# Optimization experiments

Hardware: AMD Instinct MI355X
Metric: run time of the kernel (lower is better)

## Reference

```python
import jax, jax.numpy as jnp
import numpy as np

NUM_NODE_TYPES = 8
HIDDEN = 64
D = 4
N_NODES = 100000
N_EDGES = 3200000
LN_EPS = 1e-5


def setup_inputs() -> dict:
    key = jax.random.key(0)
    ks = jax.random.split(key, 8)
    total_in = 2 * NUM_NODE_TYPES
    out_dim = D * D
    x = jax.random.normal(ks[0], (N_NODES, 16), dtype=jnp.float32)
    edge_index = jax.random.randint(ks[1], (2, N_EDGES), 0, N_NODES, dtype=jnp.int64)
    node_types = jax.random.randint(ks[2], (N_NODES,), 0, NUM_NODE_TYPES, dtype=jnp.int64)
    # LayerNorm params
    ln_g = jnp.ones((total_in,), dtype=jnp.float32)
    ln_b = jnp.zeros((total_in,), dtype=jnp.float32)
    # Linear layers (kaiming-ish init)
    W1 = jax.random.normal(ks[3], (total_in, HIDDEN), dtype=jnp.float32) * (1.0 / np.sqrt(total_in))
    b1 = jnp.zeros((HIDDEN,), dtype=jnp.float32)
    W2 = jax.random.normal(ks[4], (HIDDEN, out_dim), dtype=jnp.float32) * (1.0 / np.sqrt(HIDDEN))
    b2 = jnp.zeros((out_dim,), dtype=jnp.float32)
    return {"x": x, "edge_index": edge_index, "node_types": node_types,
            "ln_g": ln_g, "ln_b": ln_b, "W1": W1, "b1": b1, "W2": W2, "b2": b2}


def reference(x, edge_index, node_types, ln_g, ln_b, W1, b1, W2, b2):
    row, col = edge_index[0], edge_index[1]
    # one-hot node types then per-edge gather of src/tgt types
    onehot = jax.nn.one_hot(node_types, NUM_NODE_TYPES, dtype=jnp.float32)  # [N, T]
    h = jnp.concatenate([onehot[row], onehot[col]], axis=-1)  # [E, 2T]
    # LayerNorm
    mu = jnp.mean(h, axis=-1, keepdims=True)
    var = jnp.mean(jnp.square(h - mu), axis=-1, keepdims=True)
    hn = (h - mu) * jax.lax.rsqrt(var + LN_EPS) * ln_g + ln_b
    # MLP
    h1 = jax.nn.relu(hn @ W1 + b1)          # [E, HIDDEN]
    h_sheaf = (h1 @ W2 + b2).reshape(-1, D, D)  # [E, d, d]
    attention_maps = jax.nn.softmax(h_sheaf, axis=-1)
    sheaf_maps = jnp.eye(D, dtype=h_sheaf.dtype)[None] - attention_maps
    return sheaf_maps
```

## Files before the change

kernel.cpp:

```cpp
#include <hip/hip_runtime.h>
#include <math.h>

#define NUM_T   8
#define TIN     16
#define HID     64
#define OUTD    16
#define LN_EPS  1e-5f

#define N_PACK_U32  12500
#define PACK_BLOCKS 49

typedef float f32x4 __attribute__((ext_vector_type(4)));

__global__ __launch_bounds__(256) void
prep_kernel(const int* __restrict__ ntypes, int n_nodes,
            const float* __restrict__ ln_g,
            const float* __restrict__ ln_b,
            const float* __restrict__ W1,
            const float* __restrict__ b1,
            const float* __restrict__ W2,
            const float* __restrict__ b2,
            f32x4* __restrict__ table4,
            unsigned int* __restrict__ packed)
{
    const int t = threadIdx.x;

    if (blockIdx.x < PACK_BLOCKS) {
        const int g = blockIdx.x * 256 + t;
        if (g < N_PACK_U32) {
            unsigned int w = 0;
            int n0 = g * 8;
            #pragma unroll
            for (int j = 0; j < 8; ++j) {
                int n = n0 + j;
                unsigned int ty = (n < n_nodes) ? (unsigned int)ntypes[n] : 0u;
                w |= (ty & 7u) << (j * 4);
            }
            packed[g] = w;
        }
        return;
    }

    if (t >= 64) return;
    const int p  = blockIdx.x - PACK_BLOCKS;
    const int ts = p >> 3;
    const int tt = p & 7;
    const int k  = t;

    const float mu = 2.0f / 16.0f;
    float var = 0.0f;
    #pragma unroll
    for (int j = 0; j < TIN; ++j) {
        float h = (j == ts || j == (8 + tt)) ? 1.0f : 0.0f;
        float d = h - mu;
        var += d * d;
    }
    var *= (1.0f / 16.0f);
    const float inv = rsqrtf(var + LN_EPS);

    float a = b1[k];
    #pragma unroll
    for (int j = 0; j < TIN; ++j) {
        float h  = (j == ts || j == (8 + tt)) ? 1.0f : 0.0f;
        float hn = (h - mu) * inv * ln_g[j] + ln_b[j];
        a += hn * W1[j * HID + k];
    }
    a = fmaxf(a, 0.0f);

    const f32x4* W2v = (const f32x4*)W2;
    f32x4 w0 = W2v[k * 4 + 0], w1 = W2v[k * 4 + 1],
          w2 = W2v[k * 4 + 2], w3 = W2v[k * 4 + 3];

    float s[OUTD];
    #pragma unroll
    for (int i = 0; i < 4; ++i) {
        s[0 + i]  = a * w0[i];
        s[4 + i]  = a * w1[i];
        s[8 + i]  = a * w2[i];
        s[12 + i] = a * w3[i];
    }
    #pragma unroll
    for (int o = 0; o < OUTD; ++o) {
        s[o] += __shfl_xor(s[o], 1);
        s[o] += __shfl_xor(s[o], 2);
        s[o] += __shfl_xor(s[o], 4);
        s[o] += __shfl_xor(s[o], 8);
        s[o] += __shfl_xor(s[o], 16);
        s[o] += __shfl_xor(s[o], 32);
        s[o] += b2[o];
    }

    if (t < 4) {
        const int r = t;
        float s0 = s[4*r+0], s1 = s[4*r+1], s2 = s[4*r+2], s3 = s[4*r+3];
        float m  = fmaxf(fmaxf(s0, s1), fmaxf(s2, s3));
        float e0 = expf(s0 - m), e1 = expf(s1 - m),
              e2 = expf(s2 - m), e3 = expf(s3 - m);
        float rs = 1.0f / (e0 + e1 + e2 + e3);
        f32x4 outv;
        outv.x = (r == 0 ? 1.0f : 0.0f) - e0 * rs;
        outv.y = (r == 1 ? 1.0f : 0.0f) - e1 * rs;
        outv.z = (r == 2 ? 1.0f : 0.0f) - e2 * rs;
        outv.w = (r == 3 ? 1.0f : 0.0f) - e3 * rs;
        table4[p * 4 + r] = outv;
    }
}

__global__ __launch_bounds__(1024) void
scatter_edges_kernel(const int* __restrict__ row,
                     const int* __restrict__ col,
                     const unsigned int* __restrict__ packed,
                     const f32x4* __restrict__ table4,
                     f32x4* __restrict__ out4,
                     int E)
{
    __shared__ f32x4 lds_table[64 * 5];
    __shared__ unsigned int nt_lds[N_PACK_U32];

    const int t = threadIdx.x;

    if (t < 256) {
        int p = t >> 2, q = t & 3;
        lds_table[p * 5 + q] = table4[t];
    }
    {
        const uint4* s4 = (const uint4*)packed;
        uint4* d4 = (uint4*)nt_lds;
        for (int i = t; i < N_PACK_U32 / 4; i += 1024) d4[i] = s4[i];
    }
    __syncthreads();

    const int lane = t & 63;
    const int wid  = t >> 6;
    const int q    = lane & 3;
    const int sub  = lane >> 2;
    const int stride = gridDim.x * 1024;

    int base = blockIdx.x * 1024 + wid * 64;
    if (base >= E) return;

    int pair;
    {
        int e  = base + lane;
        int ec = (e < E) ? e : (E - 1);
        int r = row[ec];
        int c = col[ec];
        unsigned int tr = (nt_lds[r >> 3] >> ((r & 7) * 4)) & 7u;
        unsigned int tc = (nt_lds[c >> 3] >> ((c & 7) * 4)) & 7u;
        pair = (int)((tr << 3) | tc);
    }

    while (base < E) {
        const int nbase = base + stride;
        const bool have_next = (nbase < E);

        int rn = 0, cn = 0;
        if (have_next) {
            int en  = nbase + lane;
            int enc = (en < E) ? en : (E - 1);
            rn = row[enc];
            cn = col[enc];
        }

        #pragma unroll
        for (int j = 0; j < 4; ++j) {
            int src = j * 16 + sub;
            int pj  = __shfl(pair, src, 64);
            int ej  = base + src;
            if (ej < E) {
                out4[ej * 4 + q] = lds_table[pj * 5 + q];
            }
        }

        if (have_next) {
            unsigned int tr = (nt_lds[rn >> 3] >> ((rn & 7) * 4)) & 7u;
            unsigned int tc = (nt_lds[cn >> 3] >> ((cn & 7) * 4)) & 7u;
            pair = (int)((tr << 3) | tc);
        }
        base = nbase;
    }
}

extern "C" void kernel_launch(void* const* d_in, const int* in_sizes, int n_in,
                              void* d_out, int out_size, void* d_ws, size_t ws_size,
                              hipStream_t stream)
{
    const int*   edge_index = (const int*)d_in[1];
    const int*   ntypes     = (const int*)d_in[2];
    const float* ln_g       = (const float*)d_in[3];
    const float* ln_b       = (const float*)d_in[4];
    const float* W1         = (const float*)d_in[5];
    const float* b1         = (const float*)d_in[6];
    const float* W2         = (const float*)d_in[7];
    const float* b2         = (const float*)d_in[8];

    const int E = in_sizes[1] / 2;
    const int N = in_sizes[2];

    f32x4*        table4 = (f32x4*)d_ws;
    unsigned int* packed = (unsigned int*)((char*)d_ws + 4096);

    prep_kernel<<<PACK_BLOCKS + 64, 256, 0, stream>>>(
        ntypes, N, ln_g, ln_b, W1, b1, W2, b2, table4, packed);

    const int blocks = 512;
    scatter_edges_kernel<<<blocks, 1024, 0, stream>>>(
        edge_index, edge_index + E, packed,
        table4, (f32x4*)d_out, E);
}
```

Before: 46.23 us.

## Add vectorized exact-chunk scatter path with int4 index loads and packed pair shuffles

Adds a fast path, used when the edge count is a multiple of 256, that processes 256-edge chunks per wavefront. Row and column indices are read with int4 loads, and four type pairs are packed into one register so a single shuffle serves four edges. The path drops bounds checks, uses a 256-block grid and keeps next-chunk prefetching. The old kernel becomes a simpler generic fallback without prefetch, and the fast path depends on the edge count's divisibility.

```diff
diff --git a/kernel.cpp b/kernel.cpp
--- a/kernel.cpp
+++ b/kernel.cpp
@@ -107,12 +107,89 @@
 }
 
 __global__ __launch_bounds__(1024) void
-scatter_edges_kernel(const int* __restrict__ row,
-                     const int* __restrict__ col,
-                     const unsigned int* __restrict__ packed,
-                     const f32x4* __restrict__ table4,
-                     f32x4* __restrict__ out4,
-                     int E)
+scatter_edges_exact(const int* __restrict__ row,
+                    const int* __restrict__ col,
+                    const unsigned int* __restrict__ packed,
+                    const f32x4* __restrict__ table4,
+                    f32x4* __restrict__ out4,
+                    int nchunks)
+{
+    __shared__ f32x4 lds_table[64 * 5];
+    __shared__ unsigned int nt_lds[N_PACK_U32];
+
+    const int t = threadIdx.x;
+
+    if (t < 256) {
+        int p = t >> 2, q = t & 3;
+        lds_table[p * 5 + q] = table4[t];
+    }
+    {
+        const uint4* s4 = (const uint4*)packed;
+        uint4* d4 = (uint4*)nt_lds;
+        for (int i = t; i < N_PACK_U32 / 4; i += 1024) d4[i] = s4[i];
+    }
+    __syncthreads();
+
+    const int lane = t & 63;
+    const int wid  = t >> 6;
+    const int q        = lane & 3;
+    const int selshift = 8 * ((lane >> 2) & 3);
+    const int lhi      = lane >> 4;
+
+    const int4* row4 = (const int4*)row;
+    const int4* col4 = (const int4*)col;
+
+    int ci = blockIdx.x * 16 + wid;
+    const int stride = gridDim.x * 16;
+    if (ci >= nchunks) return;
+
+    int4 rv = row4[ci * 64 + lane];
+    int4 cv = col4[ci * 64 + lane];
+
+    while (true) {
+        const int nci = ci + stride;
+        const bool have_next = (nci < nchunks);
+
+        int4 rvn, cvn;
+        if (have_next) {
+            rvn = row4[nci * 64 + lane];
+            cvn = col4[nci * 64 + lane];
+        }
+
+        unsigned int pp = 0;
+        {
+            int rr[4] = {rv.x, rv.y, rv.z, rv.w};
+            int cc[4] = {cv.x, cv.y, cv.z, cv.w};
+            #pragma unroll
+            for (int j = 0; j < 4; ++j) {
+                unsigned int tr = (nt_lds[rr[j] >> 3] >> ((rr[j] & 7) * 4)) & 7u;
+                unsigned int tc = (nt_lds[cc[j] >> 3] >> ((cc[j] & 7) * 4)) & 7u;
+                pp |= ((tr << 3) | tc) << (8 * j);
+            }
+        }
+
+        const int base4 = ci * 1024;
+        #pragma unroll
+        for (int i = 0; i < 16; ++i) {
+            unsigned int ppj = (unsigned int)__shfl((int)pp, 4 * i + lhi, 64);
+            int pj = (int)((ppj >> selshift) & 63u);
+            out4[base4 + i * 64 + lane] = lds_table[pj * 5 + q];
+        }
+
+        if (!have_next) break;
+        ci = nci;
+        rv = rvn;
+        cv = cvn;
+    }
+}
+
+__global__ __launch_bounds__(1024) void
+scatter_edges_generic(const int* __restrict__ row,
+                      const int* __restrict__ col,
+                      const unsigned int* __restrict__ packed,
+                      const f32x4* __restrict__ table4,
+                      f32x4* __restrict__ out4,
+                      int E)
 {
     __shared__ f32x4 lds_table[64 * 5];
     __shared__ unsigned int nt_lds[N_PACK_U32];
@@ -136,48 +213,22 @@
     const int sub  = lane >> 2;
     const int stride = gridDim.x * 1024;
 
-    int base = blockIdx.x * 1024 + wid * 64;
-    if (base >= E) return;
-
-    int pair;
-    {
+    for (int base = blockIdx.x * 1024 + wid * 64; base < E; base += stride) {
         int e  = base + lane;
         int ec = (e < E) ? e : (E - 1);
         int r = row[ec];
         int c = col[ec];
         unsigned int tr = (nt_lds[r >> 3] >> ((r & 7) * 4)) & 7u;
         unsigned int tc = (nt_lds[c >> 3] >> ((c & 7) * 4)) & 7u;
-        pair = (int)((tr << 3) | tc);
-    }
-
-    while (base < E) {
-        const int nbase = base + stride;
-        const bool have_next = (nbase < E);
-
-        int rn = 0, cn = 0;
-        if (have_next) {
-            int en  = nbase + lane;
-            int enc = (en < E) ? en : (E - 1);
-            rn = row[enc];
-            cn = col[enc];
-        }
+        int pair = (int)((tr << 3) | tc);
 
         #pragma unroll
         for (int j = 0; j < 4; ++j) {
             int src = j * 16 + sub;
             int pj  = __shfl(pair, src, 64);
             int ej  = base + src;
-            if (ej < E) {
-                out4[ej * 4 + q] = lds_table[pj * 5 + q];
-            }
-        }
-
-        if (have_next) {
-            unsigned int tr = (nt_lds[rn >> 3] >> ((rn & 7) * 4)) & 7u;
-            unsigned int tc = (nt_lds[cn >> 3] >> ((cn & 7) * 4)) & 7u;
-            pair = (int)((tr << 3) | tc);
-        }
-        base = nbase;
+            if (ej < E) out4[ej * 4 + q] = lds_table[pj * 5 + q];
+        }
     }
 }
 
@@ -203,8 +254,11 @@
     prep_kernel<<<PACK_BLOCKS + 64, 256, 0, stream>>>(
         ntypes, N, ln_g, ln_b, W1, b1, W2, b2, table4, packed);
 
-    const int blocks = 512;
-    scatter_edges_kernel<<<blocks, 1024, 0, stream>>>(
-        edge_index, edge_index + E, packed,
-        table4, (f32x4*)d_out, E);
-}
+    if ((E & 255) == 0) {
+        scatter_edges_exact<<<256, 1024, 0, stream>>>(
+            edge_index, edge_index + E, packed, table4, (f32x4*)d_out, E >> 8);
+    } else {
+        scatter_edges_generic<<<512, 1024, 0, stream>>>(
+            edge_index, edge_index + E, packed, table4, (f32x4*)d_out, E);
+    }
+}
```

After: 47.02 us. About the same (+1.7%).
